# Kernel optimization log

Hardware: AMD Instinct MI355X
Metric: run time of the kernel (lower is better)

Reference implementation:

```python
import jax, jax.numpy as jnp
import numpy as np

B = 1024; K = 7; N = 32; F = 5; E = 16; CO_F = 50; CO_K = 128; CO_E = 32


def normalize(a):
    # L1 row-normalization of adjacency along last dim (source 'normalize' unavailable)
    return a / (jnp.sum(jnp.abs(a), axis=-1, keepdims=True) + 1e-6)


def se_block(x, w1, w2):  # x [B,C,N,N]
    s = x.mean(axis=(2, 3))
    g = jax.nn.sigmoid(jax.nn.relu(s @ w1) @ w2)
    return x * g[:, :, None, None]


def vq(z, cb, win, wout):  # z [B,C,N,M]; quantize projected row vectors
    ze = jnp.einsum('bcnm,me->bcne', z, win)
    flat = ze.reshape(-1, ze.shape[-1])
    d2 = (flat * flat).sum(-1, keepdims=True) - 2.0 * flat @ cb.T + (cb * cb).sum(-1)
    idx = jnp.argmin(d2, axis=-1)
    q = cb[idx].reshape(ze.shape)
    sg = jax.lax.stop_gradient
    loss = jnp.mean((sg(ze) - q) ** 2) + 0.25 * jnp.mean((ze - sg(q)) ** 2)
    zq = ze + sg(q - ze)  # straight-through
    recon = jnp.einsum('bcne,em->bcnm', zq, wout)
    return loss, recon


def cbam(x, w1, w2, cv):  # x [B,C,D]; channel attn MLP + spatial conv1d(k=7)
    avg = x.mean(axis=-1); mx = x.max(axis=-1)
    ca = jax.nn.sigmoid(jax.nn.relu(avg @ w1) @ w2 + jax.nn.relu(mx @ w1) @ w2)
    x = x * ca[:, :, None]
    s = jnp.stack([x.mean(axis=1), x.max(axis=1)], axis=1)  # [B,2,D]
    sa = jax.lax.conv_general_dilated(s, cv, (1,), [(3, 3)], dimension_numbers=('NCH', 'OIH', 'NCH'))
    return x * jax.nn.sigmoid(sa)


def get_adj_f(sf, p, bias, q, theta, sw1, sw2, cb, win, wout):
    o = jnp.einsum('ij,bjd->bid', p, sf) + bias
    g = jax.nn.elu((o @ q) @ theta)  # [B,n,n*f]
    b, n = g.shape[0], g.shape[1]
    adj = normalize(jnp.transpose(g.reshape(b, n, n, -1), (0, 3, 1, 2)))  # [B,f,n,n]
    loss, recon = vq(adj, cb, win, wout)
    ar = jax.nn.elu(se_block(recon, sw1, sw2) + recon)
    return loss, normalize(jax.nn.elu(ar.sum(axis=1)))  # [B,n,n]


def res_gcn_f(x, adj, w1, w2, a1, a2, a3, b1, b2, b3):
    x1 = jax.nn.selu(jnp.einsum('bij,bjd->bid', adj, x @ w1))
    x1 = cbam(jnp.concatenate([x, x1], axis=2), a1, a2, a3)
    x2 = jax.nn.selu(jnp.einsum('bij,bjd->bid', adj, x1 @ w2))
    return cbam(jnp.concatenate([x1, x2], axis=2), b1, b2, b3)


def res_gcn2_f(x, adj, w1, w2, a1, a2, a3, b1, b2, b3):
    x1 = jax.nn.selu(jnp.einsum('bij,bjd->bid', adj, x @ w1))
    x1 = cbam(x1, a1, a2, a3) + x1
    x2 = jax.nn.selu(jnp.einsum('bij,bjd->bid', adj, x1 @ w2))
    return cbam(x2, b1, b2, b3) + x2


def _forward(x, ga_p, ga_bias, ga_q, ga_theta, ga_se_w1, ga_se_w2, ga_cb, ga_win, ga_wout, rg_w1, rg_w2, cb1_w1, cb1_w2, cb1_conv, cb2_w1, cb2_w2, cb2_conv, co_p, co_bias, co_q, co_theta, co_se_w1, co_se_w2, co_cb, co_win, co_wout, co_rg_w1, co_rg_w2, co_cb1_w1, co_cb1_w2, co_cb1_conv, co_cb2_w1, co_cb2_w2, co_cb2_conv, W_att):
    b = x.shape[0]
    sub = jnp.transpose(x.reshape(b, K, N, F), (1, 0, 2, 3))  # [K,B,N,F] contiguous clusters
    losses, adjs = jax.vmap(get_adj_f)(sub, ga_p, ga_bias, ga_q, ga_theta, ga_se_w1, ga_se_w2, ga_cb, ga_win, ga_wout)
    xi = jax.nn.elu(jax.vmap(res_gcn_f)(sub, adjs, rg_w1, rg_w2, cb1_w1, cb1_w2, cb1_conv, cb2_w1, cb2_w2, cb2_conv))  # [K,B,N,50]
    xr = jnp.transpose(xi, (1, 0, 2, 3))  # [B,K,N,50]
    # att_coarsen per cluster -> one node per cluster
    fw = jnp.einsum('bknd,dh->bknh', xr, W_att)
    att = jnp.einsum('bknh,bkmh->bknm', fw, fw).sum(axis=-1)
    a = jax.nn.softmax(att, axis=-1)
    xc = jnp.einsum('bkn,bknd->bkd', a, xr)  # [B,K,50]
    loss_co, adj_co = get_adj_f(xc, co_p, co_bias, co_q, co_theta, co_se_w1, co_se_w2, co_cb, co_win, co_wout)
    x_co = res_gcn2_f(xc, adj_co, co_rg_w1, co_rg_w2, co_cb1_w1, co_cb1_w2, co_cb1_conv, co_cb2_w1, co_cb2_w2, co_cb2_conv)
    return losses.sum() + 2.0 * loss_co, x_co


def setup_inputs() -> dict:
    key = jax.random.key(0)
    ks = iter(jax.random.split(key, 64))
    def rn(shape, s=0.1):
        return jax.random.normal(next(ks), shape, jnp.float32) * s
    return {
        'x': jax.random.normal(next(ks), (B, K * N, F), jnp.float32),
        'ga_p': rn((K, N, N)), 'ga_bias': jnp.zeros((K, N, F), jnp.float32),
        'ga_q': rn((K, F, F)), 'ga_theta': rn((K, F, N * F)),
        'ga_se_w1': rn((K, F, 2)), 'ga_se_w2': rn((K, 2, F)),
        'ga_cb': rn((K, 32, E)), 'ga_win': rn((K, N, E)), 'ga_wout': rn((K, E, N)),
        'rg_w1': rn((K, F, F + 10)), 'rg_w2': rn((K, F + 15, F + 25)),
        'cb1_w1': rn((K, N, 8)), 'cb1_w2': rn((K, 8, N)), 'cb1_conv': rn((K, 1, 2, 7)),
        'cb2_w1': rn((K, N, 8)), 'cb2_w2': rn((K, 8, N)), 'cb2_conv': rn((K, 1, 2, 7)),
        'co_p': rn((K, K)), 'co_bias': jnp.zeros((K, CO_F), jnp.float32),
        'co_q': rn((CO_F, CO_F)), 'co_theta': rn((CO_F, K * CO_F)),
        'co_se_w1': rn((CO_F, 25)), 'co_se_w2': rn((25, CO_F)),
        'co_cb': rn((CO_K, CO_E)), 'co_win': rn((K, CO_E)), 'co_wout': rn((CO_E, K)),
        'co_rg_w1': rn((CO_F, CO_F + 5)), 'co_rg_w2': rn((CO_F + 5, CO_F + 10)),
        'co_cb1_w1': rn((K, 1)), 'co_cb1_w2': rn((1, K)), 'co_cb1_conv': rn((1, 2, 7)),
        'co_cb2_w1': rn((K, 1)), 'co_cb2_w2': rn((1, K)), 'co_cb2_conv': rn((1, 2, 7)),
        'W_att': rn((CO_F, 80)),
    }


def reference(x, ga_p, ga_bias, ga_q, ga_theta, ga_se_w1, ga_se_w2, ga_cb, ga_win, ga_wout, rg_w1, rg_w2, cb1_w1, cb1_w2, cb1_conv, cb2_w1, cb2_w2, cb2_conv, co_p, co_bias, co_q, co_theta, co_se_w1, co_se_w2, co_cb, co_win, co_wout, co_rg_w1, co_rg_w2, co_cb1_w1, co_cb1_w2, co_cb1_conv, co_cb2_w1, co_cb2_w2, co_cb2_conv, W_att):
    return _forward(x, ga_p, ga_bias, ga_q, ga_theta, ga_se_w1, ga_se_w2, ga_cb, ga_win, ga_wout, rg_w1, rg_w2, cb1_w1, cb1_w2, cb1_conv, cb2_w1, cb2_w2, cb2_conv, co_p, co_bias, co_q, co_theta, co_se_w1, co_se_w2, co_cb, co_win, co_wout, co_rg_w1, co_rg_w2, co_cb1_w1, co_cb1_w2, co_cb1_conv, co_cb2_w1, co_cb2_w2, co_cb2_conv, W_att)
```

## Files before the change

kernel.cpp:

```cpp
#include <hip/hip_runtime.h>
#include <hip/hip_bf16.h>

__device__ __forceinline__ float frcp(float x){ return __builtin_amdgcn_rcpf(x); }
__device__ __forceinline__ float eluf_p(float x){ return x > 0.f ? x : expm1f(x); }
__device__ __forceinline__ float eluf_f(float x){ return x > 0.f ? x : __expf(x)-1.f; }
__device__ __forceinline__ float seluf(float x){
  return x > 0.f ? 1.0507009873554805f*x : 1.7580993408473766f*(__expf(x)-1.f);
}
__device__ __forceinline__ float sigm(float x){ return frcp(1.f+__expf(-x)); }

__device__ __forceinline__ void cbam32(float* X, int D,
    const float* w1 , const float* w2 , const float* cv ,
    float* avgv, float* mxv, float* cav, float* smean, float* smax, float* sav,
    float* h1, float* h2, int tid)
{
  if (tid < 32){
    float s=0.f, m=-INFINITY;
    const float* row = X + tid*D;
    for (int d=0; d<D; ++d){ float v=row[d]; s+=v; m=fmaxf(m,v); }
    avgv[tid]=s/(float)D; mxv[tid]=m;
  }
  __syncthreads();
  if (tid < 8){
    float a=0.f, mm=0.f;
    for (int c=0;c<32;++c){ a += avgv[c]*w1[c*8+tid]; mm += mxv[c]*w1[c*8+tid]; }
    h1[tid]=fmaxf(a,0.f); h2[tid]=fmaxf(mm,0.f);
  }
  __syncthreads();
  if (tid < 32){
    float a=0.f;
    for (int j=0;j<8;++j) a += (h1[j]+h2[j])*w2[j*32+tid];
    cav[tid]=sigm(a);
  }
  __syncthreads();
  for (int o=tid;o<32*D;o+=256) X[o] *= cav[o/D];
  __syncthreads();
  if (tid < D){
    float s=0.f, m=-INFINITY;
    for (int c=0;c<32;++c){ float v=X[c*D+tid]; s+=v; m=fmaxf(m,v); }
    smean[tid]=s/32.f; smax[tid]=m;
  }
  __syncthreads();
  if (tid < D){
    float a=0.f;
    for (int t=0;t<7;++t){
      int dd=tid+t-3;
      if (dd>=0 && dd<D) a += cv[t]*smean[dd] + cv[7+t]*smax[dd];
    }
    sav[tid]=a;
  }
  __syncthreads();
  for (int o=tid;o<32*D;o+=256) X[o] *= sigm(sav[o%D]);
  __syncthreads();
}

#define TH(e,c)   uA[(e)*160+(c)]
#define CBS(c,e)  uA[800+(c)*16+(e)]
#define CBN(c)    uA[1312+(c)]
#define WINS(m,e) uA[1344+(m)*16+(e)]
#define WSUM(e)   uA[1856+(e)]
#define DECF(c,m) uA[1872+(c)*33+(m)]
#define X1C_BASE  (uA)
#define CAT2_BASE (uA+640)

__global__ __launch_bounds__(256, 3)
void k_fine(const float* __restrict__ x, const float* __restrict__ ga_p, const float* __restrict__ ga_bias,
            const float* __restrict__ ga_q, const float* __restrict__ ga_theta,
            const float* __restrict__ ga_se_w1, const float* __restrict__ ga_se_w2,
            const float* __restrict__ ga_cb, const float* __restrict__ ga_win, const float* __restrict__ ga_wout,
            const float* __restrict__ rg_w1, const float* __restrict__ rg_w2,
            const float* __restrict__ cb1_w1, const float* __restrict__ cb1_w2, const float* __restrict__ cb1_cv,
            const float* __restrict__ cb2_w1, const float* __restrict__ cb2_w2, const float* __restrict__ cb2_cv,
            float* __restrict__ xr, float* __restrict__ lossAcc)
{
  const int tid = threadIdx.x;
  const int blk = blockIdx.x;
  const int k = blk >> 10;
  const int b = blk & 1023;

  __shared__ float uA[2928];
  __shared__ float sf[32][5];
  __shared__ float qm[5][5];
  __shared__ float sw1[5][2];
  __shared__ float sw2[2][5];
  __shared__ float w1g[5][15];
  __shared__ float w2g[20][30];
  __shared__ float c1w1[32][8]; __shared__ float c1w2[8][32]; __shared__ float c1cv[14];
  __shared__ float c2w1[32][8]; __shared__ float c2w2[8][32]; __shared__ float c2cv[14];
  __shared__ float o_[32][5];
  __shared__ float oqS[32][5];
  __shared__ int   idxv[160];
  __shared__ float gse[5];
  __shared__ float wredS[5];
  __shared__ float adjFT[32][32];
  __shared__ float xw[32][30];
  __shared__ float avgv[32], mxv[32], cav[32];
  __shared__ float smean[50], smax[50], sav[50];
  __shared__ float h1s[8], h2s[8];
  __shared__ float ssew[4];

  {
    const float* xs = x + (size_t)(b*224 + k*32)*5;
    for (int i = tid; i < 160; i += 256) ((float*)sf)[i]    = xs[i];
    for (int i = tid; i < 25;  i += 256) ((float*)qm)[i]    = ga_q[k*25 + i];
    for (int i = tid; i < 800; i += 256) uA[i]              = ga_theta[k*800 + i];
    for (int i = tid; i < 10;  i += 256) ((float*)sw1)[i]   = ga_se_w1[k*10 + i];
    for (int i = tid; i < 10;  i += 256) ((float*)sw2)[i]   = ga_se_w2[k*10 + i];
    for (int i = tid; i < 512; i += 256) uA[800+i]          = ga_cb[k*512 + i];
    for (int i = tid; i < 512; i += 256) uA[1344+i]         = ga_win[k*512 + i];
    for (int i = tid; i < 75;  i += 256) ((float*)w1g)[i]   = rg_w1[k*75 + i];
    for (int i = tid; i < 600; i += 256) ((float*)w2g)[i]   = rg_w2[k*600 + i];
    for (int i = tid; i < 256; i += 256) ((float*)c1w1)[i]  = cb1_w1[k*256 + i];
    for (int i = tid; i < 256; i += 256) ((float*)c1w2)[i]  = cb1_w2[k*256 + i];
    for (int i = tid; i < 14;  i += 256) c1cv[i]            = cb1_cv[k*14 + i];
    for (int i = tid; i < 256; i += 256) ((float*)c2w1)[i]  = cb2_w1[k*256 + i];
    for (int i = tid; i < 256; i += 256) ((float*)c2w2)[i]  = cb2_w2[k*256 + i];
    for (int i = tid; i < 14;  i += 256) c2cv[i]            = cb2_cv[k*14 + i];
  }
  __syncthreads();

  if (tid < 160){
    int i = tid/5, d = tid%5;
    const float* pk = ga_p + k*1024 + i*32;
    float a = ga_bias[k*160 + tid];
    for (int j=0;j<32;++j) a += pk[j] * sf[j][d];
    o_[i][d] = a;
  } else if (tid < 176){
    int e = tid - 160;
    const float* wg = ga_wout + k*512 + e*32;
    float s = 0.f;
    #pragma unroll
    for (int m=0;m<32;++m) s += wg[m];
    WSUM(e) = s;
  } else if (tid >= 224){
    int c = tid - 224;
    float s = 0.f;
    #pragma unroll
    for (int e=0;e<16;++e){ float v = CBS(c,e); s += v*v; }
    CBN(c) = s;
  }
  __syncthreads();
  if (tid < 160){
    int i = tid/5, e = tid%5;
    float a = 0.f;
    #pragma unroll
    for (int d=0;d<5;++d) a += o_[i][d]*qm[d][e];
    oqS[i][e] = a;
  }
  __syncthreads();

  float sse = 0.f;
  if (tid < 160){
    const int f = tid >> 5, i = tid & 31;
    const float oq0=oqS[i][0], oq1=oqS[i][1], oq2=oqS[i][2], oq3=oqS[i][3], oq4=oqS[i][4];
    float v[16];
    #pragma unroll
    for (int e=0;e<16;++e) v[e] = 0.f;
    float s1 = 0.f;
    #pragma unroll 4
    for (int m=0;m<32;++m){
      const int c = m*5+f;
      float a = oq0*TH(0,c) + oq1*TH(1,c) + oq2*TH(2,c) + oq3*TH(3,c) + oq4*TH(4,c);
      a = eluf_p(a);
      s1 += fabsf(a);
      #pragma unroll
      for (int e=0;e<16;++e) v[e] += a*WINS(m,e);
    }
    const float inv = 1.f/(s1 + 1e-6f);
    #pragma unroll
    for (int e=0;e<16;++e) v[e] *= inv;
    float vv = 0.f;
    #pragma unroll
    for (int e=0;e<16;++e) vv += v[e]*v[e];
    float best = 3.4e38f; int bi = 0;
    #pragma unroll 4
    for (int c=0;c<32;++c){
      float d = 0.f;
      #pragma unroll
      for (int e=0;e<16;++e) d += v[e]*CBS(c,e);
      float d2 = vv - 2.f*d + CBN(c);
      if (d2 < best){ best = d2; bi = c; }
    }
    idxv[tid] = bi;
    sse = best;
  } else {
    for (int o = tid-160; o < 480; o += 96){
      int j = o/15, c = o%15;
      float a = 0.f;
      #pragma unroll
      for (int d=0;d<5;++d) a += sf[j][d]*w1g[d][c];
      xw[j][c] = a;
    }
    const float* wg = ga_wout + k*512;
    for (int o = tid-160; o < 1024; o += 96){
      int c = o >> 5, m = o & 31;
      float a = 0.f;
      #pragma unroll
      for (int e=0;e<16;++e) a += CBS(c,e)*wg[e*32+m];
      DECF(c,m) = a;
    }
  }
  __syncthreads();

  {
    float sep = 0.f;
    if (tid < 160){
      const int id = idxv[tid];
      #pragma unroll
      for (int e=0;e<16;++e) sep += CBS(id,e)*WSUM(e);
    }
    #pragma unroll
    for (int off=16; off>=1; off>>=1) sep += __shfl_xor(sep, off);
    if (tid < 160 && (tid&31)==0) wredS[tid>>5] = sep;
  }
  __syncthreads();
  if (tid == 0){
    float h0=0.f, h1=0.f;
    #pragma unroll
    for (int f=0; f<5; ++f){
      float s = wredS[f] * (1.f/1024.f);
      h0 += s*sw1[f][0]; h1 += s*sw1[f][1];
    }
    h0 = fmaxf(h0,0.f); h1 = fmaxf(h1,0.f);
    #pragma unroll
    for (int f=0; f<5; ++f) gse[f] = sigm(h0*sw2[0][f] + h1*sw2[1][f]);
  }
  __syncthreads();

  for (int o = tid; o < 1024; o += 256){
    int i = o & 31, m = o >> 5;
    float a = 0.f;
    #pragma unroll
    for (int f=0; f<5; ++f)
      a += eluf_f(DECF(idxv[(f<<5)|i], m)*(1.f+gse[f]));
    adjFT[m][i] = eluf_f(a);
  }
  __syncthreads();
  if (tid < 32){
    float s = 0.f;
    #pragma unroll
    for (int m=0;m<32;++m) s += fabsf(adjFT[m][tid]);
    float inv = 1.f/(s + 1e-6f);
    #pragma unroll
    for (int m=0;m<32;++m) adjFT[m][tid] *= inv;
  }
  __syncthreads();

  float* x1c = X1C_BASE;
  for (int o = tid; o < 480; o += 256){
    int i = o/15, c = o%15;
    float a = 0.f;
    for (int j=0;j<32;++j) a += adjFT[j][i]*xw[j][c];
    x1c[i*20 + 5+c] = seluf(a);
  }
  for (int o = tid; o < 160; o += 256) x1c[(o/5)*20 + o%5] = ((const float*)sf)[o];
  __syncthreads();
  cbam32(x1c, 20, &c1w1[0][0], &c1w2[0][0], c1cv,
         avgv, mxv, cav, smean, smax, sav, h1s, h2s, tid);

  float* cat2 = CAT2_BASE;
  for (int o = tid; o < 960; o += 256){
    int j = o/30, c = o%30;
    float a = 0.f;
    #pragma unroll
    for (int d=0;d<20;++d) a += x1c[j*20+d]*w2g[d][c];
    xw[j][c] = a;
  }
  __syncthreads();
  for (int o = tid; o < 960; o += 256){
    int i = o/30, c = o%30;
    float a = 0.f;
    for (int j=0;j<32;++j) a += adjFT[j][i]*xw[j][c];
    cat2[i*50 + 20+c] = seluf(a);
  }
  for (int o = tid; o < 640; o += 256) cat2[(o/20)*50 + o%20] = x1c[o];
  __syncthreads();
  cbam32(cat2, 50, &c2w1[0][0], &c2w2[0][0], c2cv,
         avgv, mxv, cav, smean, smax, sav, h1s, h2s, tid);

  {
    float* dst = xr + (size_t)(b*7 + k)*1600;
    for (int o = tid; o < 1600; o += 256) dst[o] = eluf_f(cat2[o]);
  }

  {
    float p = sse;
    for (int off=32; off>=1; off>>=1) p += __shfl_down(p, off);
    if ((tid & 63) == 0) ssew[tid>>6] = p;
  }
  __syncthreads();
  if (tid == 0)
    atomicAdd(lossAcc, (ssew[0]+ssew[1]+ssew[2]+ssew[3]) * (1.25f/2621440.f));
}

__global__ __launch_bounds__(256)
void k_attco(const float* __restrict__ xr, const float* __restrict__ Watt,
             const float* __restrict__ co_p, const float* __restrict__ co_bias,
             const float* __restrict__ co_q, const float* __restrict__ co_theta,
             const float* __restrict__ co_sew1, const float* __restrict__ co_sew2,
             const float* __restrict__ co_cb, const float* __restrict__ co_win, const float* __restrict__ co_wout,
             const float* __restrict__ co_w1, const float* __restrict__ co_w2,
             const float* __restrict__ cc1w1, const float* __restrict__ cc1w2, const float* __restrict__ cc1cv,
             const float* __restrict__ cc2w1, const float* __restrict__ cc2w2, const float* __restrict__ cc2cv,
             float* __restrict__ outp, float* __restrict__ lossAcc)
{
  const int b = blockIdx.x, tid = threadIdx.x;
  const int lane = tid & 63, wid = tid >> 6;
  __shared__ float uB[2368];
  __shared__ float xc[7][50];
  __shared__ float pm[7][7];
  __shared__ float o_[7][50];
  __shared__ float oqS[7][50];
  __shared__ float adjZ[50][7][7];
  __shared__ float winS[7][32];
  __shared__ float woutS[32][7];
  __shared__ float cbS[128][33];
  __shared__ float decC[128][8];
  __shared__ int   idxv[350];
  __shared__ float s_se[50], hh[25], gse[50];
  __shared__ float adjA[49];
  __shared__ float adjco[7][7];
  __shared__ float cw1a[7], cw2a[7], cva[14], cw1b[7], cw2b[7], cvb[14];
  __shared__ float avgv[7], mxv[7], cav[7], smean[60], smax[60], sav[60];
  __shared__ float hsum[1];
  __shared__ float ssew[4];

  float* attU  = &cbS[0][0];
  float* M_    = attU;
  float* S_    = attU + 350;
  float* T_    = attU + 910;
  float* attS_ = attU + 1260;
  float* aw_   = attU + 1484;

  for (int i = tid; i < 49;   i += 256) ((float*)pm)[i]    = co_p[i];
  for (int i = tid; i < 224;  i += 256) ((float*)winS)[i]  = co_win[i];
  for (int i = tid; i < 224;  i += 256) ((float*)woutS)[i] = co_wout[i];
  if (tid < 7)                       cw1a[tid]     = cc1w1[tid];
  else if (tid >= 32 && tid < 39)    cw2a[tid-32]  = cc1w2[tid-32];
  else if (tid >= 64 && tid < 78)    cva[tid-64]   = cc1cv[tid-64];
  else if (tid >= 96 && tid < 103)   cw1b[tid-96]  = cc2w1[tid-96];
  else if (tid >= 128 && tid < 135)  cw2b[tid-128] = cc2w2[tid-128];
  else if (tid >= 160 && tid < 174)  cvb[tid-160]  = cc2cv[tid-160];

  const float* src = xr + (size_t)b*11200;
  for (int o = tid; o < 350; o += 256){
    int kk = o/50, d = o%50;
    float s = 0.f;
    const float* p = src + kk*1600 + d;
    for (int n=0;n<32;++n) s += p[n*50];
    M_[kk*50+d] = s;
  }
  __syncthreads();
  for (int o = tid; o < 560; o += 256){
    int kk = o/80, h = o%80;
    float s = 0.f;
    #pragma unroll 8
    for (int d=0;d<50;++d) s += M_[kk*50+d]*Watt[d*80+h];
    S_[kk*80+h] = s;
  }
  __syncthreads();
  for (int o = tid; o < 350; o += 256){
    int kk = o/50, d = o%50;
    float s = 0.f;
    const float* wr = Watt + d*80;
    #pragma unroll 8
    for (int h=0;h<80;++h) s += S_[kk*80+h]*wr[h];
    T_[kk*50+d] = s;
  }
  __syncthreads();
  for (int o = tid; o < 224; o += 256){
    int kk = o >> 5, n = o & 31;
    float s = 0.f;
    const float* p = src + kk*1600 + n*50;
    #pragma unroll 8
    for (int d=0;d<50;++d) s += p[d]*T_[kk*50+d];
    attS_[kk*32+n] = s;
  }
  __syncthreads();
  if (tid < 7){
    float m = -INFINITY;
    for (int n=0;n<32;++n) m = fmaxf(m, attS_[tid*32+n]);
    float s = 0.f;
    for (int n=0;n<32;++n){ float e = expf(attS_[tid*32+n]-m); aw_[tid*32+n] = e; s += e; }
    for (int n=0;n<32;++n) aw_[tid*32+n] = aw_[tid*32+n]/s;
  }
  __syncthreads();
  for (int o = tid; o < 350; o += 256){
    int kk = o/50, d = o%50;
    float s = 0.f;
    const float* p = src + kk*1600 + d;
    for (int n=0;n<32;++n) s += aw_[kk*32+n]*p[n*50];
    xc[kk][d] = s;
  }
  __syncthreads();

  for (int i = tid; i < 4096; i += 256) cbS[i>>5][i&31] = co_cb[i];
  for (int o = tid; o < 350; o += 256){
    int i = o/50, d = o%50;
    float a = co_bias[o];
    #pragma unroll
    for (int j=0;j<7;++j) a += pm[i][j]*xc[j][d];
    o_[i][d] = a;
  }
  __syncthreads();
  for (int o = tid; o < 350; o += 256){
    int i = o/50, e = o%50;
    float a = 0.f;
    #pragma unroll 8
    for (int d=0;d<50;++d) a += o_[i][d]*co_q[d*50+e];
    oqS[i][e] = a;
  }
  __syncthreads();
  for (int c = tid; c < 350; c += 256){
    float acc[7] = {0,0,0,0,0,0,0};
    #pragma unroll 5
    for (int e=0;e<50;++e){
      float t = co_theta[e*350+c];
      #pragma unroll
      for (int i=0;i<7;++i) acc[i] += oqS[i][e]*t;
    }
    int f = c % 50, n2 = c / 50;
    #pragma unroll
    for (int i=0;i<7;++i) adjZ[f][i][n2] = eluf_p(acc[i]);
  }
  __syncthreads();
  for (int o = tid; o < 350; o += 256){
    float* rowp = &adjZ[0][0][0] + o*7;
    float s = 0.f;
    #pragma unroll
    for (int m=0;m<7;++m) s += fabsf(rowp[m]);
    float den = s + 1e-6f;
    #pragma unroll
    for (int m=0;m<7;++m) rowp[m] /= den;
  }
  __syncthreads();

  float c0[32], c1[32];
  #pragma unroll
  for (int e=0;e<32;++e){ c0[e] = cbS[lane][e]; c1[e] = cbS[lane+64][e]; }
  float cn0 = 0.f, cn1 = 0.f;
  #pragma unroll
  for (int e=0;e<32;++e){ cn0 += c0[e]*c0[e]; cn1 += c1[e]*c1[e]; }
  float* zeG = uB;
  float* vvG = uB + 2304;
  float sse = 0.f;
  for (int g0 = 0; g0 < 350; g0 += 64){
    int nv = (350 - g0 < 64) ? (350 - g0) : 64;
    for (int o = tid; o < nv*32; o += 256){
      int v = o >> 5, e = o & 31;
      const float* rowp = &adjZ[0][0][0] + (g0+v)*7;
      float a = 0.f;
      #pragma unroll
      for (int m=0;m<7;++m) a += rowp[m]*winS[m][e];
      zeG[v*36+e] = a;
    }
    __syncthreads();
    if (tid < nv){
      float a = 0.f;
      #pragma unroll
      for (int e=0;e<32;++e){ float t = zeG[tid*36+e]; a += t*t; }
      vvG[tid] = a;
    }
    __syncthreads();
    for (int v = wid; v < nv; v += 4){
      float d0 = 0.f, d1 = 0.f;
      #pragma unroll
      for (int e=0;e<32;++e){
        float ve = zeG[v*36+e];
        d0 += ve*c0[e]; d1 += ve*c1[e];
      }
      float vv = vvG[v];
      float dist0 = vv - 2.f*d0 + cn0;
      float dist1 = vv - 2.f*d1 + cn1;
      float best = dist0; int bi = lane;
      if (dist1 < best){ best = dist1; bi = lane + 64; }
      for (int off = 32; off >= 1; off >>= 1){
        float ob = __shfl_xor(best, off);
        int oi   = __shfl_xor(bi, off);
        if (ob < best || (ob == best && oi < bi)){ best = ob; bi = oi; }
      }
      if (lane == 0){ idxv[g0+v] = bi; sse += best; }
    }
    __syncthreads();
  }

  for (int o = tid; o < 896; o += 256){
    int c = o / 7, m = o % 7;
    float a = 0.f;
    #pragma unroll
    for (int e=0;e<32;++e) a += cbS[c][e]*woutS[e][m];
    decC[c][m] = a;
  }
  __syncthreads();
  for (int o = tid; o < 2450; o += 256){
    int fr = o / 49, r = o % 49, i = r / 7, m = r % 7;
    (&adjZ[0][0][0])[o] = decC[idxv[fr*7 + i]][m];
  }
  __syncthreads();
  const float* reconC = &adjZ[0][0][0];

  if (tid < 50){
    float s = 0.f;
    for (int r=0;r<49;++r) s += reconC[tid*49 + r];
    s_se[tid] = s / 49.f;
  }
  __syncthreads();
  if (tid < 25){
    float a = 0.f;
    #pragma unroll 8
    for (int f=0;f<50;++f) a += s_se[f]*co_sew1[f*25+tid];
    hh[tid] = fmaxf(a, 0.f);
  }
  __syncthreads();
  if (tid < 50){
    float a = 0.f;
    #pragma unroll 8
    for (int t2=0;t2<25;++t2) a += hh[t2]*co_sew2[t2*50+tid];
    gse[tid] = sigm(a);
  }
  __syncthreads();
  if (tid < 49){
    float a = 0.f;
    for (int f=0;f<50;++f) a += eluf_f(reconC[f*49+tid]*(1.f+gse[f]));
    adjA[tid] = eluf_f(a);
  }
  __syncthreads();
  if (tid < 7){
    float s = 0.f;
    #pragma unroll
    for (int m=0;m<7;++m) s += fabsf(adjA[tid*7+m]);
    float den = s + 1e-6f;
    #pragma unroll
    for (int m=0;m<7;++m) adjco[tid][m] = adjA[tid*7+m]/den;
  }
  __syncthreads();

  float* x1w = uB;
  float* x1s = uB + 385;
  float* x1b = uB + 770;
  float* xw2 = uB + 1155;
  float* x2s = uB + 1575;
  for (int o = tid; o < 385; o += 256){
    int j = o/55, c = o%55;
    float a = 0.f;
    #pragma unroll 8
    for (int d=0;d<50;++d) a += xc[j][d]*co_w1[d*55+c];
    x1w[o] = a;
  }
  __syncthreads();
  for (int o = tid; o < 385; o += 256){
    int i = o/55, c = o%55;
    float a = 0.f;
    #pragma unroll
    for (int j=0;j<7;++j) a += adjco[i][j]*x1w[j*55+c];
    x1s[o] = seluf(a);
  }
  __syncthreads();
  if (tid < 7){
    float s=0.f, m=-INFINITY;
    for (int d=0;d<55;++d){ float v = x1s[tid*55+d]; s += v; m = fmaxf(m,v); }
    avgv[tid] = s/55.f; mxv[tid] = m;
  }
  __syncthreads();
  if (tid == 0){
    float ha=0.f, hm=0.f;
    #pragma unroll
    for (int c=0;c<7;++c){ ha += avgv[c]*cw1a[c]; hm += mxv[c]*cw1a[c]; }
    hsum[0] = fmaxf(ha,0.f) + fmaxf(hm,0.f);
  }
  __syncthreads();
  if (tid < 7) cav[tid] = sigm(hsum[0]*cw2a[tid]);
  __syncthreads();
  for (int o = tid; o < 385; o += 256) x1w[o] = x1s[o]*cav[o/55];
  __syncthreads();
  if (tid < 55){
    float s=0.f, m=-INFINITY;
    #pragma unroll
    for (int c=0;c<7;++c){ float v = x1w[c*55+tid]; s += v; m = fmaxf(m,v); }
    smean[tid] = s/7.f; smax[tid] = m;
  }
  __syncthreads();
  if (tid < 55){
    float a = 0.f;
    #pragma unroll
    for (int t2=0;t2<7;++t2){
      int dd = tid + t2 - 3;
      if (dd >= 0 && dd < 55) a += cva[t2]*smean[dd] + cva[7+t2]*smax[dd];
    }
    sav[tid] = a;
  }
  __syncthreads();
  for (int o = tid; o < 385; o += 256)
    x1b[o] = x1w[o]*sigm(sav[o%55]) + x1s[o];
  __syncthreads();

  for (int o = tid; o < 420; o += 256){
    int j = o/60, c = o%60;
    float a = 0.f;
    #pragma unroll 8
    for (int d=0;d<55;++d) a += x1b[j*55+d]*co_w2[d*60+c];
    xw2[o] = a;
  }
  __syncthreads();
  for (int o = tid; o < 420; o += 256){
    int i = o/60, c = o%60;
    float a = 0.f;
    #pragma unroll
    for (int j=0;j<7;++j) a += adjco[i][j]*xw2[j*60+c];
    x2s[o] = seluf(a);
  }
  __syncthreads();
  if (tid < 7){
    float s=0.f, m=-INFINITY;
    for (int d=0;d<60;++d){ float v = x2s[tid*60+d]; s += v; m = fmaxf(m,v); }
    avgv[tid] = s/60.f; mxv[tid] = m;
  }
  __syncthreads();
  if (tid == 0){
    float ha=0.f, hm=0.f;
    #pragma unroll
    for (int c=0;c<7;++c){ ha += avgv[c]*cw1b[c]; hm += mxv[c]*cw1b[c]; }
    hsum[0] = fmaxf(ha,0.f) + fmaxf(hm,0.f);
  }
  __syncthreads();
  if (tid < 7) cav[tid] = sigm(hsum[0]*cw2b[tid]);
  __syncthreads();
  for (int o = tid; o < 420; o += 256) xw2[o] = x2s[o]*cav[o/60];
  __syncthreads();
  if (tid < 60){
    float s=0.f, m=-INFINITY;
    #pragma unroll
    for (int c=0;c<7;++c){ float v = xw2[c*60+tid]; s += v; m = fmaxf(m,v); }
    smean[tid] = s/7.f; smax[tid] = m;
  }
  __syncthreads();
  if (tid < 60){
    float a = 0.f;
    #pragma unroll
    for (int t2=0;t2<7;++t2){
      int dd = tid + t2 - 3;
      if (dd >= 0 && dd < 60) a += cvb[t2]*smean[dd] + cvb[7+t2]*smax[dd];
    }
    sav[tid] = a;
  }
  __syncthreads();
  for (int o = tid; o < 420; o += 256){
    float val = xw2[o]*sigm(sav[o%60]) + x2s[o];
    outp[1 + (size_t)b*420 + o] = val;
  }

  if (lane == 0) ssew[wid] = sse;
  __syncthreads();
  if (tid == 0)
    atomicAdd(lossAcc, (ssew[0]+ssew[1]+ssew[2]+ssew[3]) * (2.5f/11468800.f));
}

__global__ void k_loss(const float* __restrict__ lossAcc, float* __restrict__ outp){
  if (threadIdx.x == 0 && blockIdx.x == 0) outp[0] = lossAcc[0];
}

extern "C" void kernel_launch(void* const* d_in, const int* in_sizes, int n_in,
                              void* d_out, int out_size, void* d_ws, size_t ws_size,
                              hipStream_t stream)
{
  const float* x          = (const float*)d_in[0];
  const float* ga_p       = (const float*)d_in[1];
  const float* ga_bias    = (const float*)d_in[2];
  const float* ga_q       = (const float*)d_in[3];
  const float* ga_theta   = (const float*)d_in[4];
  const float* ga_se_w1   = (const float*)d_in[5];
  const float* ga_se_w2   = (const float*)d_in[6];
  const float* ga_cb      = (const float*)d_in[7];
  const float* ga_win     = (const float*)d_in[8];
  const float* ga_wout    = (const float*)d_in[9];
  const float* rg_w1      = (const float*)d_in[10];
  const float* rg_w2      = (const float*)d_in[11];
  const float* cb1_w1     = (const float*)d_in[12];
  const float* cb1_w2     = (const float*)d_in[13];
  const float* cb1_conv   = (const float*)d_in[14];
  const float* cb2_w1     = (const float*)d_in[15];
  const float* cb2_w2     = (const float*)d_in[16];
  const float* cb2_conv   = (const float*)d_in[17];
  const float* co_p       = (const float*)d_in[18];
  const float* co_bias    = (const float*)d_in[19];
  const float* co_q       = (const float*)d_in[20];
  const float* co_theta   = (const float*)d_in[21];
  const float* co_se_w1   = (const float*)d_in[22];
  const float* co_se_w2   = (const float*)d_in[23];
  const float* co_cb      = (const float*)d_in[24];
  const float* co_win     = (const float*)d_in[25];
  const float* co_wout    = (const float*)d_in[26];
  const float* co_rg_w1   = (const float*)d_in[27];
  const float* co_rg_w2   = (const float*)d_in[28];
  const float* co_cb1_w1  = (const float*)d_in[29];
  const float* co_cb1_w2  = (const float*)d_in[30];
  const float* co_cb1_cv  = (const float*)d_in[31];
  const float* co_cb2_w1  = (const float*)d_in[32];
  const float* co_cb2_w2  = (const float*)d_in[33];
  const float* co_cb2_cv  = (const float*)d_in[34];
  const float* W_att      = (const float*)d_in[35];

  char* base = (char*)d_ws;
  float* lossAcc = (float*)base;
  float* xr  = (float*)(base + 256);

  float* outp = (float*)d_out;

  hipMemsetAsync(d_ws, 0, 256, stream);
  k_fine<<<7168, 256, 0, stream>>>(x, ga_p, ga_bias, ga_q, ga_theta, ga_se_w1, ga_se_w2,
                                   ga_cb, ga_win, ga_wout, rg_w1, rg_w2,
                                   cb1_w1, cb1_w2, cb1_conv, cb2_w1, cb2_w2, cb2_conv,
                                   xr, lossAcc);
  k_attco<<<1024, 256, 0, stream>>>(xr, W_att, co_p, co_bias, co_q, co_theta,
                                    co_se_w1, co_se_w2, co_cb, co_win, co_wout,
                                    co_rg_w1, co_rg_w2,
                                    co_cb1_w1, co_cb1_w2, co_cb1_cv,
                                    co_cb2_w1, co_cb2_w2, co_cb2_cv,
                                    outp, lossAcc);
  k_loss<<<1, 64, 0, stream>>>(lossAcc, outp);
}
```

Baseline: 499.7 us.

## Replace wave-parallel VQ argmin with per-thread codebook scan in k_attco

The co-attention VQ step no longer stages the codebook in LDS with each wave covering all 128 codes through per-lane registers and shuffle reductions. Each thread now handles one of the 350 projected rows, computes its 32-dim embedding in registers and scans all 128 codes directly from global memory, using code norms precomputed in shared memory. Codebook norms and the decoder table are now computed earlier, overlapping the adjacency stage, and the LDS footprint shrinks. In exchange only 350 of 512 thread slots do work (in two passes), each doing a serial 128x32 scan through global/cache loads, and the loss sum now needs a wave reduction.

New measurement: 600.3 us. +20.1%, slower.

```diff
diff --git a/kernel.cpp b/kernel.cpp
--- a/kernel.cpp
+++ b/kernel.cpp
@@ -306,7 +306,7 @@
 {
   const int b = blockIdx.x, tid = threadIdx.x;
   const int lane = tid & 63, wid = tid >> 6;
-  __shared__ float uB[2368];
+  __shared__ float uB[2000];
   __shared__ float xc[7][50];
   __shared__ float pm[7][7];
   __shared__ float o_[7][50];
@@ -314,7 +314,7 @@
   __shared__ float adjZ[50][7][7];
   __shared__ float winS[7][32];
   __shared__ float woutS[32][7];
-  __shared__ float cbS[128][33];
+  __shared__ float cbn[128];
   __shared__ float decC[128][8];
   __shared__ int   idxv[350];
   __shared__ float s_se[50], hh[25], gse[50];
@@ -325,12 +325,11 @@
   __shared__ float hsum[1];
   __shared__ float ssew[4];
 
-  float* attU  = &cbS[0][0];
-  float* M_    = attU;
-  float* S_    = attU + 350;
-  float* T_    = attU + 910;
-  float* attS_ = attU + 1260;
-  float* aw_   = attU + 1484;
+  float* M_    = uB;
+  float* S_    = uB + 350;
+  float* T_    = uB + 910;
+  float* attS_ = uB + 1260;
+  float* aw_   = uB + 1484;
 
   for (int i = tid; i < 49;   i += 256) ((float*)pm)[i]    = co_p[i];
   for (int i = tid; i < 224;  i += 256) ((float*)winS)[i]  = co_win[i];
@@ -394,7 +393,6 @@
   }
   __syncthreads();
 
-  for (int i = tid; i < 4096; i += 256) cbS[i>>5][i&31] = co_cb[i];
   for (int o = tid; o < 350; o += 256){
     int i = o/50, d = o%50;
     float a = co_bias[o];
@@ -423,6 +421,21 @@
     #pragma unroll
     for (int i=0;i<7;++i) adjZ[f][i][n2] = eluf_p(acc[i]);
   }
+  if (tid < 128){
+    const float* cr = co_cb + tid*32;
+    float s = 0.f;
+    #pragma unroll
+    for (int e=0;e<32;++e) s += cr[e]*cr[e];
+    cbn[tid] = s;
+  }
+  for (int o = tid; o < 896; o += 256){
+    int c = o / 7, m = o % 7;
+    const float* cr = co_cb + c*32;
+    float a = 0.f;
+    #pragma unroll
+    for (int e=0;e<32;++e) a += cr[e]*woutS[e][m];
+    decC[c][m] = a;
+  }
   __syncthreads();
   for (int o = tid; o < 350; o += 256){
     float* rowp = &adjZ[0][0][0] + o*7;
@@ -435,65 +448,40 @@
   }
   __syncthreads();
 
-  float c0[32], c1[32];
-  #pragma unroll
-  for (int e=0;e<32;++e){ c0[e] = cbS[lane][e]; c1[e] = cbS[lane+64][e]; }
-  float cn0 = 0.f, cn1 = 0.f;
-  #pragma unroll
-  for (int e=0;e<32;++e){ cn0 += c0[e]*c0[e]; cn1 += c1[e]*c1[e]; }
-  float* zeG = uB;
-  float* vvG = uB + 2304;
   float sse = 0.f;
-  for (int g0 = 0; g0 < 350; g0 += 64){
-    int nv = (350 - g0 < 64) ? (350 - g0) : 64;
-    for (int o = tid; o < nv*32; o += 256){
-      int v = o >> 5, e = o & 31;
-      const float* rowp = &adjZ[0][0][0] + (g0+v)*7;
+  for (int v = tid; v < 350; v += 256){
+    const float* rowp = &adjZ[0][0][0] + v*7;
+    float r[7];
+    #pragma unroll
+    for (int m=0;m<7;++m) r[m] = rowp[m];
+    float ze[32];
+    #pragma unroll
+    for (int e=0;e<32;++e){
       float a = 0.f;
       #pragma unroll
-      for (int m=0;m<7;++m) a += rowp[m]*winS[m][e];
-      zeG[v*36+e] = a;
-    }
-    __syncthreads();
-    if (tid < nv){
-      float a = 0.f;
+      for (int m=0;m<7;++m) a += r[m]*winS[m][e];
+      ze[e] = a;
+    }
+    float vv = 0.f;
+    #pragma unroll
+    for (int e=0;e<32;++e) vv += ze[e]*ze[e];
+    float best = 3.4e38f; int bi = 0;
+    #pragma unroll 4
+    for (int c=0;c<128;++c){
+      const float* cr = co_cb + c*32;
+      float d = 0.f;
       #pragma unroll
-      for (int e=0;e<32;++e){ float t = zeG[tid*36+e]; a += t*t; }
-      vvG[tid] = a;
-    }
-    __syncthreads();
-    for (int v = wid; v < nv; v += 4){
-      float d0 = 0.f, d1 = 0.f;
-      #pragma unroll
-      for (int e=0;e<32;++e){
-        float ve = zeG[v*36+e];
-        d0 += ve*c0[e]; d1 += ve*c1[e];
-      }
-      float vv = vvG[v];
-      float dist0 = vv - 2.f*d0 + cn0;
-      float dist1 = vv - 2.f*d1 + cn1;
-      float best = dist0; int bi = lane;
-      if (dist1 < best){ best = dist1; bi = lane + 64; }
-      for (int off = 32; off >= 1; off >>= 1){
-        float ob = __shfl_xor(best, off);
-        int oi   = __shfl_xor(bi, off);
-        if (ob < best || (ob == best && oi < bi)){ best = ob; bi = oi; }
-      }
-      if (lane == 0){ idxv[g0+v] = bi; sse += best; }
-    }
-    __syncthreads();
-  }
-
-  for (int o = tid; o < 896; o += 256){
-    int c = o / 7, m = o % 7;
-    float a = 0.f;
-    #pragma unroll
-    for (int e=0;e<32;++e) a += cbS[c][e]*woutS[e][m];
-    decC[c][m] = a;
-  }
-  __syncthreads();
+      for (int e=0;e<32;++e) d += ze[e]*cr[e];
+      float d2 = vv - 2.f*d + cbn[c];
+      if (d2 < best){ best = d2; bi = c; }
+    }
+    idxv[v] = bi;
+    sse += best;
+  }
+  __syncthreads();
+
   for (int o = tid; o < 2450; o += 256){
-    int fr = o / 49, r = o % 49, i = r / 7, m = r % 7;
+    int fr = o / 49, r2 = o % 49, i = r2 / 7, m = r2 % 7;
     (&adjZ[0][0][0])[o] = decC[idxv[fr*7 + i]][m];
   }
   __syncthreads();
@@ -501,7 +489,7 @@
 
   if (tid < 50){
     float s = 0.f;
-    for (int r=0;r<49;++r) s += reconC[tid*49 + r];
+    for (int r2=0;r2<49;++r2) s += reconC[tid*49 + r2];
     s_se[tid] = s / 49.f;
   }
   __syncthreads();
@@ -649,7 +637,11 @@
     outp[1 + (size_t)b*420 + o] = val;
   }
 
-  if (lane == 0) ssew[wid] = sse;
+  {
+    float p = sse;
+    for (int off=32; off>=1; off>>=1) p += __shfl_down(p, off);
+    if (lane == 0) ssew[wid] = p;
+  }
   __syncthreads();
   if (tid == 0)
     atomicAdd(lossAcc, (ssew[0]+ssew[1]+ssew[2]+ssew[3]) * (2.5f/11468800.f));
```
